# Optimization experiments

Hardware: AMD Instinct MI355X
Metric: run time of the kernel (lower is better)

## Reference

```python
import jax, jax.numpy as jnp
import numpy as np
from jax import lax

BITS = 8  # w_p = a_p = 8 (HAWQ int8)

def _round_ste(x):
    # straight-through round (quant-aware training semantics)
    return x + lax.stop_gradient(jnp.round(x) - x)

def _quant_act(x):
    # QuantAct: symmetric per-tensor activation fake-quant; returns (quantized x, scale)
    n = 2.0 ** (BITS - 1) - 1.0
    sf = jnp.maximum(jnp.max(jnp.abs(x)) / n, 1e-8)
    q = jnp.clip(_round_ste(x / sf), -n, n)
    return q * sf, sf

def _quant_conv(x, w, b, pre_sf, stride, pad):
    # QuantConv2d: per-output-channel symmetric weight quant, integer conv on
    # x/pre_sf with rounded weights, rescale by pre_sf * w_sf. Bias quantized at
    # combined scale. Returns (float output, w_sf) for scale propagation.
    n = 2.0 ** (BITS - 1) - 1.0
    w_sf = jnp.maximum(jnp.max(jnp.abs(w), axis=(1, 2, 3)) / n, 1e-8)
    w_int = _round_ste(w / w_sf[:, None, None, None])
    b_sf = w_sf * pre_sf
    b_int = _round_ste(b / b_sf)
    y = lax.conv_general_dilated(x / pre_sf, w_int, (stride, stride),
                                 [(pad, pad), (pad, pad)],
                                 dimension_numbers=('NCHW', 'OIHW', 'NCHW'))
    return (y + b_int[None, :, None, None]) * b_sf[None, :, None, None], w_sf

def _bn(x, g, b, m, v, eps=1e-5):
    # BatchNorm2d in eval mode (running stats), folded into scale/shift
    inv = g / jnp.sqrt(v + eps)
    return x * inv[None, :, None, None] + (b - m * inv)[None, :, None, None]

def _quant_linear(x, w, b, pre_sf):
    # QuantLinear: per-output-row symmetric weight quant
    n = 2.0 ** (BITS - 1) - 1.0
    w_sf = jnp.maximum(jnp.max(jnp.abs(w), axis=1) / n, 1e-8)
    w_int = _round_ste(w / w_sf[:, None])
    b_sf = w_sf * pre_sf
    b_int = _round_ste(b / b_sf)
    return ((x / pre_sf) @ w_int.T + b_int[None, :]) * b_sf[None, :]

def _forward(x, w0, b0, g0, bb0, m0, v0, w1, b1, g1, bb1, m1, v1,
             w2, b2, g2, bb2, m2, v2, w3, b3, g3, bb3, m3, v3,
             w4, b4, g4, bb4, m4, v4, wd, bd):
    x, psf = _quant_act(x)
    x, _ = _quant_conv(x, w0, b0, psf, 1, 1)   # [B,32,32,32]
    x = _bn(x, g0, bb0, m0, v0)
    x, psf = _quant_act(x)
    x, _ = _quant_conv(x, w1, b1, psf, 1, 0)   # 1x1 -> [B,4,32,32]
    x = _bn(x, g1, bb1, m1, v1)
    x, psf = _quant_act(x)
    x, _ = _quant_conv(x, w2, b2, psf, 2, 1)   # [B,32,16,16]
    x = _bn(x, g2, bb2, m2, v2)
    x, psf = _quant_act(x)
    x, _ = _quant_conv(x, w3, b3, psf, 2, 1)   # [B,32,8,8]
    x = _bn(x, g3, bb3, m3, v3)
    x, psf = _quant_act(x)
    x, _ = _quant_conv(x, w4, b4, psf, 1, 1)   # [B,32,8,8]
    x = _bn(x, g4, bb4, m4, v4)
    x, psf = _quant_act(x)
    x = x.reshape(-1, 2048)                    # 32*8*8 = 2048
    x = _quant_linear(x, wd, bd, psf)          # [B,10]
    return jax.nn.softmax(x, axis=0)           # dim=0 as in original module

def setup_inputs() -> dict:
    key = jax.random.key(0)
    ks = jax.random.split(key, 40)
    B = 1024
    inp = {"x": jax.random.normal(ks[0], (B, 3, 32, 32), jnp.float32)}
    conv_shapes = [(32, 3, 3, 3), (4, 32, 1, 1), (32, 4, 3, 3), (32, 32, 3, 3), (32, 32, 3, 3)]
    for i, s in enumerate(conv_shapes):
        c = s[0]
        inp[f"w{i}"] = jax.random.normal(ks[1 + i], s, jnp.float32) * 0.1
        inp[f"b{i}"] = jax.random.normal(ks[6 + i], (c,), jnp.float32) * 0.01
        inp[f"g{i}"] = 1.0 + 0.1 * jax.random.normal(ks[11 + i], (c,), jnp.float32)
        inp[f"bb{i}"] = 0.1 * jax.random.normal(ks[16 + i], (c,), jnp.float32)
        inp[f"m{i}"] = 0.1 * jax.random.normal(ks[21 + i], (c,), jnp.float32)
        inp[f"v{i}"] = 0.5 + jax.random.uniform(ks[26 + i], (c,), jnp.float32)
    inp["wd"] = jax.random.normal(ks[31], (10, 2048), jnp.float32) * 0.05
    inp["bd"] = jnp.zeros((10,), jnp.float32)
    return inp

def reference(x, w0, b0, g0, bb0, m0, v0, w1, b1, g1, bb1, m1, v1,
              w2, b2, g2, bb2, m2, v2, w3, b3, g3, bb3, m3, v3,
              w4, b4, g4, bb4, m4, v4, wd, bd):
    return _forward(x, w0, b0, g0, bb0, m0, v0, w1, b1, g1, bb1, m1, v1,
                    w2, b2, g2, bb2, m2, v2, w3, b3, g3, bb3, m3, v3,
                    w4, b4, g4, bb4, m4, v4, wd, bd)
```

## Files before the change

kernel.cpp:

```cpp
#include <hip/hip_runtime.h>

#define DI __device__ __forceinline__

constexpr int OFF_W0KT = 384;
constexpr int OFF_W0P  = 1248;
constexpr int OFF_W1I  = 2144;
constexpr int OFF_W2KT = 2272;
constexpr int OFF_W3T  = 3424;
constexpr int OFF_W4T  = 13792;
constexpr int OFF_WDI  = 24160;
constexpr int OFF_WSF0 = 44640;
constexpr int OFF_BNS0 = 44672;
constexpr int OFF_BNB0 = 44704;
constexpr int OFF_WSF1 = 44736;
constexpr int OFF_BNS1 = 44740;
constexpr int OFF_BNB1 = 44744;
constexpr int OFF_WSF2 = 44748;
constexpr int OFF_BNS2 = 44780;
constexpr int OFF_BNB2 = 44812;
constexpr int OFF_WSF3 = 44844;
constexpr int OFF_BNS3 = 44876;
constexpr int OFF_BNB3 = 44908;
constexpr int OFF_WSF4 = 44940;
constexpr int OFF_BNS4 = 44972;
constexpr int OFF_BNB4 = 45004;
constexpr int OFF_WSFD = 45036;
constexpr int OFF_LOG  = 45056;
constexpr int OFF_ACT  = 55296;
constexpr long ACT_A_OFF = OFF_ACT;
constexpr long ACT_B_OFF = OFF_ACT + 8388608L;

DI float quantm(float x, float rsf) {
    float q = rintf(x * rsf);
    return fminf(fmaxf(q, -127.0f), 127.0f);
}
DI float get_sf(const unsigned* umax, int slot) {
    const unsigned* p = umax + slot * 64;
    unsigned m = 0u;
    #pragma unroll
    for (int i = 0; i < 64; ++i) m = m > p[i] ? m : p[i];
    return fmaxf(__uint_as_float(m) / 127.0f, 1e-8f);
}
DI void block_max_atomic(float v, unsigned* dst) {
    __shared__ float redm_[4];
    #pragma unroll
    for (int o = 32; o; o >>= 1) v = fmaxf(v, __shfl_down(v, o, 64));
    int wid = threadIdx.x >> 6;
    if ((threadIdx.x & 63) == 0) redm_[wid] = v;
    __syncthreads();
    if (threadIdx.x == 0) {
        int nw = blockDim.x >> 6;
        float m = redm_[0];
        for (int i = 1; i < nw; ++i) m = fmaxf(m, redm_[i]);
        atomicMax(dst + (blockIdx.x & 63), __float_as_uint(m));
    }
}

struct PrepEntry {
    const float *w, *g, *bb, *m, *v;
    float *wsf, *dst, *dst2, *bns, *bnb;
    int K; int has_bn; int mode;
};
struct PrepAll { PrepEntry e[6]; unsigned* umax; };

__global__ __launch_bounds__(256) void k_prep_all(PrepAll pa) {
    int blk = blockIdx.x;
    if (blk == 142) {
        for (int i = threadIdx.x; i < 384; i += 256) pa.umax[i] = 0u;
        return;
    }
    int layer, oc;
    if      (blk < 32)  { layer = 0; oc = blk; }
    else if (blk < 36)  { layer = 1; oc = blk - 32; }
    else if (blk < 68)  { layer = 2; oc = blk - 36; }
    else if (blk < 100) { layer = 3; oc = blk - 68; }
    else if (blk < 132) { layer = 4; oc = blk - 100; }
    else                { layer = 5; oc = blk - 132; }
    PrepEntry a = pa.e[layer];
    const float* wr = a.w + (long)oc * a.K;
    float mx = 0.f;
    for (int i = threadIdx.x; i < a.K; i += 256) mx = fmaxf(mx, fabsf(wr[i]));
    __shared__ float red[4];
    __shared__ float s_sf;
    #pragma unroll
    for (int o = 32; o; o >>= 1) mx = fmaxf(mx, __shfl_down(mx, o, 64));
    if ((threadIdx.x & 63) == 0) red[threadIdx.x >> 6] = mx;
    __syncthreads();
    if (threadIdx.x == 0) {
        float t = fmaxf(fmaxf(red[0], red[1]), fmaxf(red[2], red[3]));
        t = fmaxf(t / 127.0f, 1e-8f);
        a.wsf[oc] = t; s_sf = t;
        if (a.has_bn) {
            float inv = a.g[oc] / sqrtf(a.v[oc] + 1e-5f);
            a.bns[oc] = inv;
            a.bnb[oc] = a.bb[oc] - a.m[oc] * inv;
        }
    }
    __syncthreads();
    float sf = s_sf;
    for (int i = threadIdx.x; i < a.K; i += 256) {
        float q = rintf(wr[i] / sf);
        if (a.mode == 0) {
            a.dst[(long)oc * a.K + i] = q;
        } else if (a.mode == 1) {
            a.dst[i * 32 + oc] = q;
        } else if (a.mode == 2) {
            a.dst[i * 32 + oc] = q;
            a.dst2[oc * 28 + i] = q;
        } else {
            int ph = i / 72, kk = i - ph * 72;
            a.dst[ph * 2592 + kk * 36 + oc] = q;
        }
    }
    if (a.mode == 2 && threadIdx.x == 0) a.dst2[oc * 28 + 27] = 0.f;
}

__global__ __launch_bounds__(256) void k_absmax(const float4* __restrict__ x, int n4, unsigned* dst) {
    float m = 0.f;
    for (int i = blockIdx.x * blockDim.x + threadIdx.x; i < n4; i += gridDim.x * blockDim.x) {
        float4 t = x[i];
        m = fmaxf(m, fmaxf(fmaxf(fabsf(t.x), fabsf(t.y)), fmaxf(fabsf(t.z), fabsf(t.w))));
    }
    block_max_atomic(m, dst);
}

__global__ __launch_bounds__(256) void k_conv0maxN(
    const float* __restrict__ x, const float* __restrict__ w0kt,
    const float* __restrict__ wsf0, const float* __restrict__ bias0,
    const float* __restrict__ bns0, const float* __restrict__ bnb0,
    const unsigned* __restrict__ umax, unsigned* __restrict__ mout) {
    __shared__ float tile[3 * 18 * 36];
    __shared__ float wlds[27 * 32];
    __shared__ float As[32], Cs[32];
    const int b  = blockIdx.x >> 1;
    const int r0 = (blockIdx.x & 1) * 16;
    const int tid = threadIdx.x;
    const float sfx = get_sf(umax, 0);
    const float rsfx = 1.0f / sfx;
    if (tid < 32) {
        int oc = tid;
        float bsf = wsf0[oc] * sfx;
        float bint = rintf(bias0[oc] / bsf);
        float a = bsf * bns0[oc];
        As[oc] = a;
        Cs[oc] = fmaf(bint, a, bnb0[oc]);
    }
    for (int i = tid; i < 1944; i += 256) tile[i] = 0.f;
    if (tid < 216) ((float4*)wlds)[tid] = ((const float4*)w0kt)[tid];
    __syncthreads();
    const float* xb = x + (long)b * 3072;
    for (int i = tid; i < 1728; i += 256) {
        int ci = i / 576, rem = i - ci * 576;
        int rr = rem >> 5, cc = rem & 31;
        int gr = r0 - 1 + rr;
        if ((unsigned)gr < 32u)
            tile[ci * 648 + rr * 36 + cc + 1] = quantm(xb[ci * 1024 + gr * 32 + cc], rsfx);
    }
    __syncthreads();
    const int oc0  = (tid >> 5) * 4;
    const int pxg  = tid & 31;
    const int row  = pxg >> 1;
    const int wcol = (pxg & 1) * 16;
    float acc[4][16];
    #pragma unroll
    for (int o = 0; o < 4; ++o)
        #pragma unroll
        for (int p = 0; p < 16; ++p) acc[o][p] = 0.f;
    #pragma unroll
    for (int kk = 0; kk < 9; ++kk) {
        int ci = kk / 3, ky = kk - ci * 3;
        const float* rp = tile + ci * 648 + (row + ky) * 36 + wcol;
        float wn[20];
        #pragma unroll
        for (int d = 0; d < 5; ++d) *(float4*)&wn[4 * d] = *(const float4*)&rp[4 * d];
        #pragma unroll
        for (int kx = 0; kx < 3; ++kx) {
            float4 wv = *(const float4*)&wlds[(kk * 3 + kx) * 32 + oc0];
            const float* wf = &wv.x;
            #pragma unroll
            for (int o = 0; o < 4; ++o)
                #pragma unroll
                for (int p = 0; p < 16; ++p)
                    acc[o][p] = fmaf(wn[p + kx], wf[o], acc[o][p]);
        }
    }
    float lmax = 0.f;
    #pragma unroll
    for (int o = 0; o < 4; ++o) {
        float A = As[oc0 + o], C = Cs[oc0 + o];
        #pragma unroll
        for (int p = 0; p < 16; ++p)
            lmax = fmaxf(lmax, fabsf(fmaf(acc[o][p], A, C)));
    }
    block_max_atomic(lmax, mout);
}

__global__ __launch_bounds__(256) void k_conv01n(
    const float* __restrict__ x, const float* __restrict__ w0p,
    const float* __restrict__ wsf0, const float* __restrict__ bias0,
    const float* __restrict__ bns0, const float* __restrict__ bnb0,
    const float* __restrict__ w1i,
    const float* __restrict__ wsf1, const float* __restrict__ bias1,
    const float* __restrict__ bns1, const float* __restrict__ bnb1,
    const unsigned* __restrict__ umax, unsigned* __restrict__ mout,
    float* __restrict__ out) {
    __shared__ float tile[3672];
    __shared__ float wls0[896];
    __shared__ float wls1[128];
    __shared__ float Aq[32], Cq[32];
    __shared__ float A1s[4], C1s[4];
    const int b   = blockIdx.x;
    const int tid = threadIdx.x;
    const float sfx = get_sf(umax, 0);
    const float rsfx = 1.0f / sfx;
    const float sf1 = get_sf(umax, 1);
    const float rsf1 = 1.0f / sf1;
    if (tid < 32) {
        int oc = tid;
        float bsf = wsf0[oc] * sfx;
        float bint = rintf(bias0[oc] / bsf);
        float a = bsf * bns0[oc];
        float c = fmaf(bint, a, bnb0[oc]);
        Aq[oc] = a * rsf1;
        Cq[oc] = c * rsf1;
    }
    if (tid >= 64 && tid < 68) {
        int oc = tid - 64;
        float bsf = wsf1[oc] * sf1;
        float bint = rintf(bias1[oc] / bsf);
        float a = bsf * bns1[oc];
        A1s[oc] = a;
        C1s[oc] = fmaf(bint, a, bnb1[oc]);
    }
    for (int i = tid; i < 3672; i += 256) tile[i] = 0.f;
    if (tid < 224) ((float4*)wls0)[tid] = ((const float4*)w0p)[tid];
    if (tid >= 128 && tid < 256) {
        int j = tid - 128;
        wls1[(j & 31) * 4 + (j >> 5)] = w1i[j];
    }
    __syncthreads();
    const float* xb = x + (long)b * 3072;
    for (int i = tid; i < 3072; i += 256) {
        int ci = i >> 10, px = i & 1023;
        int iy = px >> 5, ix = px & 31;
        tile[ci * 1224 + (iy + 1) * 36 + (ix + 1)] = quantm(xb[i], rsfx);
    }
    __syncthreads();
    const int h   = tid >> 3;
    const int w0c = (tid & 7) * 4;
    float win[3][3][6];
    #pragma unroll
    for (int ci = 0; ci < 3; ++ci)
        #pragma unroll
        for (int ky = 0; ky < 3; ++ky) {
            const int base = ci * 1224 + (h + ky) * 36 + w0c;
            *(float4*)&win[ci][ky][0] = *(const float4*)&tile[base];
            *(float2*)&win[ci][ky][4] = *(const float2*)&tile[base + 4];
        }
    float acc1[4][4];
    #pragma unroll
    for (int o = 0; o < 4; ++o)
        #pragma unroll
        for (int p = 0; p < 4; ++p) acc1[o][p] = 0.f;
    #pragma unroll 2
    for (int oc = 0; oc < 32; ++oc) {
        float wreg[28];
        const float4* wp4 = (const float4*)&wls0[oc * 28];
        #pragma unroll
        for (int d = 0; d < 7; ++d) *(float4*)&wreg[4 * d] = wp4[d];
        float a0 = 0.f, a1 = 0.f, a2 = 0.f, a3 = 0.f;
        #pragma unroll
        for (int ci = 0; ci < 3; ++ci)
            #pragma unroll
            for (int ky = 0; ky < 3; ++ky)
                #pragma unroll
                for (int kx = 0; kx < 3; ++kx) {
                    float wv = wreg[ci * 9 + ky * 3 + kx];
                    a0 = fmaf(win[ci][ky][kx + 0], wv, a0);
                    a1 = fmaf(win[ci][ky][kx + 1], wv, a1);
                    a2 = fmaf(win[ci][ky][kx + 2], wv, a2);
                    a3 = fmaf(win[ci][ky][kx + 3], wv, a3);
                }
        float A = Aq[oc], C = Cq[oc];
        float q0 = fminf(fmaxf(rintf(fmaf(a0, A, C)), -127.0f), 127.0f);
        float q1 = fminf(fmaxf(rintf(fmaf(a1, A, C)), -127.0f), 127.0f);
        float q2 = fminf(fmaxf(rintf(fmaf(a2, A, C)), -127.0f), 127.0f);
        float q3 = fminf(fmaxf(rintf(fmaf(a3, A, C)), -127.0f), 127.0f);
        const float4 w1v = *(const float4*)&wls1[oc * 4];
        acc1[0][0] = fmaf(q0, w1v.x, acc1[0][0]); acc1[0][1] = fmaf(q1, w1v.x, acc1[0][1]);
        acc1[0][2] = fmaf(q2, w1v.x, acc1[0][2]); acc1[0][3] = fmaf(q3, w1v.x, acc1[0][3]);
        acc1[1][0] = fmaf(q0, w1v.y, acc1[1][0]); acc1[1][1] = fmaf(q1, w1v.y, acc1[1][1]);
        acc1[1][2] = fmaf(q2, w1v.y, acc1[1][2]); acc1[1][3] = fmaf(q3, w1v.y, acc1[1][3]);
        acc1[2][0] = fmaf(q0, w1v.z, acc1[2][0]); acc1[2][1] = fmaf(q1, w1v.z, acc1[2][1]);
        acc1[2][2] = fmaf(q2, w1v.z, acc1[2][2]); acc1[2][3] = fmaf(q3, w1v.z, acc1[2][3]);
        acc1[3][0] = fmaf(q0, w1v.w, acc1[3][0]); acc1[3][1] = fmaf(q1, w1v.w, acc1[3][1]);
        acc1[3][2] = fmaf(q2, w1v.w, acc1[3][2]); acc1[3][3] = fmaf(q3, w1v.w, acc1[3][3]);
    }
    float lmax = 0.f;
    float* ob = out + (long)b * 4096 + h * 32 + w0c;
    #pragma unroll
    for (int o = 0; o < 4; ++o) {
        float y0 = fmaf(acc1[o][0], A1s[o], C1s[o]);
        float y1 = fmaf(acc1[o][1], A1s[o], C1s[o]);
        float y2 = fmaf(acc1[o][2], A1s[o], C1s[o]);
        float y3 = fmaf(acc1[o][3], A1s[o], C1s[o]);
        lmax = fmaxf(lmax, fmaxf(fmaxf(fabsf(y0), fabsf(y1)), fmaxf(fabsf(y2), fabsf(y3))));
        float4 r4; r4.x = y0; r4.y = y1; r4.z = y2; r4.w = y3;
        *(float4*)&ob[o * 1024] = r4;
    }
    block_max_atomic(lmax, mout);
}

__global__ __launch_bounds__(256) void k_conv2c(
    const float* __restrict__ inp, const float* __restrict__ w2kt,
    const float* __restrict__ wsf, const float* __restrict__ bias,
    const float* __restrict__ bns, const float* __restrict__ bnb,
    const unsigned* __restrict__ umax, unsigned* __restrict__ mout,
    float* __restrict__ out) {
    __shared__ float tile[4 * 34 * 36];
    __shared__ float wlds[36 * 32];
    __shared__ float As[32], Cs[32];
    const int tid = threadIdx.x;
    const float sf = get_sf(umax, 2);
    const float rsf = 1.0f / sf;
    if (tid < 32) {
        int oc = tid;
        float bsf = wsf[oc] * sf;
        float bint = rintf(bias[oc] / bsf);
        float a = bsf * bns[oc];
        As[oc] = a;
        Cs[oc] = fmaf(bint, a, bnb[oc]);
    }
    for (int i = tid; i < 4896; i += 256) tile[i] = 0.f;
    for (int i = tid; i < 288; i += 256) ((float4*)wlds)[i] = ((const float4*)w2kt)[i];
    __syncthreads();
    const float* ib = inp + (long)blockIdx.x * 4096;
    for (int i = tid; i < 4096; i += 256) {
        int ci = i >> 10, px = i & 1023;
        int iy = px >> 5, ix = px & 31;
        tile[ci * 1224 + (iy + 1) * 36 + (ix + 1)] = quantm(ib[i], rsf);
    }
    __syncthreads();
    const int oc0 = (tid >> 6) * 8;
    const int pxq = tid & 63;
    const int h = pxq >> 2, c = pxq & 3;
    float acc[8][4];
    #pragma unroll
    for (int k = 0; k < 8; ++k)
        #pragma unroll
        for (int p = 0; p < 4; ++p) acc[k][p] = 0.f;
    #pragma unroll
    for (int ci = 0; ci < 4; ++ci) {
        #pragma unroll
        for (int ky = 0; ky < 3; ++ky) {
            const float* rp = tile + ci * 1224 + (2 * h + ky) * 36 + 8 * c;
            float wn[12];
            #pragma unroll
            for (int d = 0; d < 3; ++d) *(float4*)&wn[4 * d] = *(const float4*)&rp[4 * d];
            #pragma unroll
            for (int kx = 0; kx < 3; ++kx) {
                const float* wp = &wlds[(ci * 9 + ky * 3 + kx) * 32 + oc0];
                float4 wa = *(const float4*)&wp[0];
                float4 wb = *(const float4*)&wp[4];
                float wf[8] = {wa.x, wa.y, wa.z, wa.w, wb.x, wb.y, wb.z, wb.w};
                #pragma unroll
                for (int k = 0; k < 8; ++k)
                    #pragma unroll
                    for (int p = 0; p < 4; ++p)
                        acc[k][p] = fmaf(wn[2 * p + kx], wf[k], acc[k][p]);
            }
        }
    }
    float lmax = 0.f;
    float* ob = out + (long)blockIdx.x * 8192;
    #pragma unroll
    for (int k = 0; k < 8; ++k) {
        int oc = oc0 + k;
        float A = As[oc], C = Cs[oc];
        float4 r;
        float* rp = &r.x;
        #pragma unroll
        for (int p = 0; p < 4; ++p) {
            float y = fmaf(acc[k][p], A, C);
            rp[p] = y;
            lmax = fmaxf(lmax, fabsf(y));
        }
        *(float4*)&ob[oc * 256 + h * 16 + c * 4] = r;
    }
    block_max_atomic(lmax, mout);
}

template<int HIN, int S>
__global__ __launch_bounds__(256) void k_conv34d(
    const float* __restrict__ inp, const float* __restrict__ wt,
    const float* __restrict__ wsf, const float* __restrict__ bias,
    const float* __restrict__ bns, const float* __restrict__ bnb,
    const unsigned* __restrict__ umax, int slot, unsigned* __restrict__ mout,
    float* __restrict__ out) {
    constexpr int ROWS = HIN + 2;
    constexpr int RS   = (S == 2) ? 20 : 12;
    constexpr int TI   = 8 * ROWS * RS;
    constexpr int PIX  = HIN * HIN;
    constexpr int PSH  = (HIN == 16) ? 8 : 6;
    constexpr int HSH  = (HIN == 16) ? 4 : 3;
    constexpr int NELT = 2 * 8 * PIX;
    constexpr int WINW = (S == 2) ? 12 : 8;
    constexpr int ND   = (S == 2) ? 3 : 2;
    __shared__ float tile[2 * TI];
    __shared__ float wlds[2592];
    __shared__ float As[32], Cs[32];
    const int tid  = threadIdx.x;
    const int imgl = tid >> 7;
    const int ocg  = (tid >> 4) & 7;
    const int pxq  = tid & 15;
    const int h = pxq >> 1, c = pxq & 1;
    const float sf = get_sf(umax, slot);
    const float rsf = 1.0f / sf;
    if (tid < 32) {
        int oc = tid;
        float bsf = wsf[oc] * sf;
        float bint = rintf(bias[oc] / bsf);
        float a = bsf * bns[oc];
        As[oc] = a;
        Cs[oc] = fmaf(bint, a, bnb[oc]);
    }
    for (int i = tid; i < 2 * TI; i += 256) tile[i] = 0.f;
    float acc[4][4];
    #pragma unroll
    for (int k = 0; k < 4; ++k)
        #pragma unroll
        for (int p = 0; p < 4; ++p) acc[k][p] = 0.f;
    const float* ib = inp + (long)blockIdx.x * 2 * 32 * PIX;
    const float4* wt4 = (const float4*)wt;
    for (int ph = 0; ph < 4; ++ph) {
        __syncthreads();
        for (int i = tid; i < NELT; i += 256) {
            int im = i >> (PSH + 3);
            int ci = (i >> PSH) & 7;
            int px = i & (PIX - 1);
            int iy = px >> HSH, ix = px & (HIN - 1);
            tile[im * TI + ci * (ROWS * RS) + (iy + 1) * RS + (ix + 1)] =
                quantm(ib[(long)((im * 32 + ph * 8 + ci) << PSH) + px], rsf);
        }
        for (int i = tid; i < 648; i += 256) ((float4*)wlds)[i] = wt4[ph * 648 + i];
        __syncthreads();
        const int tbo = imgl * TI;
        #pragma unroll
        for (int ci = 0; ci < 8; ++ci) {
            float win[3][WINW];
            #pragma unroll
            for (int ky = 0; ky < 3; ++ky) {
                const int base = tbo + ci * (ROWS * RS) + (S * h + ky) * RS + S * 4 * c;
                #pragma unroll
                for (int d = 0; d < ND; ++d)
                    *(float4*)&win[ky][4 * d] = *(const float4*)&tile[base + 4 * d];
            }
            #pragma unroll
            for (int ky = 0; ky < 3; ++ky)
                #pragma unroll
                for (int kx = 0; kx < 3; ++kx) {
                    int j = ky * 3 + kx;
                    float4 wv = *(const float4*)&wlds[(ci * 9 + j) * 36 + ocg * 4];
                    float x0 = win[ky][S * 0 + kx];
                    float x1 = win[ky][S * 1 + kx];
                    float x2 = win[ky][S * 2 + kx];
                    float x3 = win[ky][S * 3 + kx];
                    acc[0][0] = fmaf(x0, wv.x, acc[0][0]); acc[0][1] = fmaf(x1, wv.x, acc[0][1]);
                    acc[0][2] = fmaf(x2, wv.x, acc[0][2]); acc[0][3] = fmaf(x3, wv.x, acc[0][3]);
                    acc[1][0] = fmaf(x0, wv.y, acc[1][0]); acc[1][1] = fmaf(x1, wv.y, acc[1][1]);
                    acc[1][2] = fmaf(x2, wv.y, acc[1][2]); acc[1][3] = fmaf(x3, wv.y, acc[1][3]);
                    acc[2][0] = fmaf(x0, wv.z, acc[2][0]); acc[2][1] = fmaf(x1, wv.z, acc[2][1]);
                    acc[2][2] = fmaf(x2, wv.z, acc[2][2]); acc[2][3] = fmaf(x3, wv.z, acc[2][3]);
                    acc[3][0] = fmaf(x0, wv.w, acc[3][0]); acc[3][1] = fmaf(x1, wv.w, acc[3][1]);
                    acc[3][2] = fmaf(x2, wv.w, acc[3][2]); acc[3][3] = fmaf(x3, wv.w, acc[3][3]);
                }
        }
    }
    float lmax = 0.f;
    long imgg = (long)blockIdx.x * 2 + imgl;
    #pragma unroll
    for (int k = 0; k < 4; ++k) {
        int oc = ocg * 4 + k;
        float A = As[oc], C = Cs[oc];
        float y0 = fmaf(acc[k][0], A, C);
        float y1 = fmaf(acc[k][1], A, C);
        float y2 = fmaf(acc[k][2], A, C);
        float y3 = fmaf(acc[k][3], A, C);
        lmax = fmaxf(lmax, fmaxf(fmaxf(fabsf(y0), fabsf(y1)), fmaxf(fabsf(y2), fabsf(y3))));
        float4 r4; r4.x = y0; r4.y = y1; r4.z = y2; r4.w = y3;
        *(float4*)&out[(imgg * 32 + oc) * 64 + h * 8 + c * 4] = r4;
    }
    block_max_atomic(lmax, mout);
}

__global__ __launch_bounds__(256) void k_fc(
    const float* __restrict__ act, const float* __restrict__ wdi,
    const float* __restrict__ wsfd, const float* __restrict__ bd,
    const unsigned* __restrict__ umax, float* __restrict__ logits) {
    int b = blockIdx.x;
    float sf = get_sf(umax, 5);
    float rsf = 1.0f / sf;
    const float* ab = act + (long)b * 2048;
    float acc[10];
    #pragma unroll
    for (int c = 0; c < 10; ++c) acc[c] = 0.f;
    #pragma unroll
    for (int k = 0; k < 8; ++k) {
        int j = threadIdx.x + 256 * k;
        float q = quantm(ab[j], rsf);
        #pragma unroll
        for (int c = 0; c < 10; ++c) acc[c] = fmaf(q, wdi[c * 2048 + j], acc[c]);
    }
    #pragma unroll
    for (int c = 0; c < 10; ++c)
        #pragma unroll
        for (int o = 32; o; o >>= 1) acc[c] += __shfl_down(acc[c], o, 64);
    __shared__ float red[4][10];
    int wid = threadIdx.x >> 6;
    if ((threadIdx.x & 63) == 0)
        #pragma unroll
        for (int c = 0; c < 10; ++c) red[wid][c] = acc[c];
    __syncthreads();
    if (threadIdx.x < 10) {
        int c = threadIdx.x;
        float s = red[0][c] + red[1][c] + red[2][c] + red[3][c];
        float bsf = wsfd[c] * sf;
        float bint = rintf(bd[c] / bsf);
        logits[b * 10 + c] = (s + bint) * bsf;
    }
}

__global__ __launch_bounds__(256) void k_softmax(const float* __restrict__ logits, float* __restrict__ out) {
    int c = blockIdx.x;
    float v0 = logits[(threadIdx.x +   0) * 10 + c];
    float v1 = logits[(threadIdx.x + 256) * 10 + c];
    float v2 = logits[(threadIdx.x + 512) * 10 + c];
    float v3 = logits[(threadIdx.x + 768) * 10 + c];
    float mx = fmaxf(fmaxf(v0, v1), fmaxf(v2, v3));
    __shared__ float redm[4];
    __shared__ float reds[4];
    #pragma unroll
    for (int o = 32; o; o >>= 1) mx = fmaxf(mx, __shfl_down(mx, o, 64));
    if ((threadIdx.x & 63) == 0) redm[threadIdx.x >> 6] = mx;
    __syncthreads();
    mx = fmaxf(fmaxf(redm[0], redm[1]), fmaxf(redm[2], redm[3]));
    float e0 = expf(v0 - mx), e1 = expf(v1 - mx), e2 = expf(v2 - mx), e3 = expf(v3 - mx);
    float s = (e0 + e1) + (e2 + e3);
    #pragma unroll
    for (int o = 32; o; o >>= 1) s += __shfl_down(s, o, 64);
    if ((threadIdx.x & 63) == 0) reds[threadIdx.x >> 6] = s;
    __syncthreads();
    s = reds[0] + reds[1] + reds[2] + reds[3];
    out[(threadIdx.x +   0) * 10 + c] = e0 / s;
    out[(threadIdx.x + 256) * 10 + c] = e1 / s;
    out[(threadIdx.x + 512) * 10 + c] = e2 / s;
    out[(threadIdx.x + 768) * 10 + c] = e3 / s;
}

extern "C" void kernel_launch(void* const* d_in, const int* in_sizes, int n_in,
                              void* d_out, int out_size, void* d_ws, size_t ws_size,
                              hipStream_t stream) {
    (void)in_sizes; (void)n_in; (void)out_size; (void)ws_size;
    const float* x = (const float*)d_in[0];
    const float *w[5], *bia[5], *g[5], *bb[5], *m[5], *v[5];
    for (int i = 0; i < 5; ++i) {
        w[i]   = (const float*)d_in[1 + 6 * i + 0];
        bia[i] = (const float*)d_in[1 + 6 * i + 1];
        g[i]   = (const float*)d_in[1 + 6 * i + 2];
        bb[i]  = (const float*)d_in[1 + 6 * i + 3];
        m[i]   = (const float*)d_in[1 + 6 * i + 4];
        v[i]   = (const float*)d_in[1 + 6 * i + 5];
    }
    const float* wd = (const float*)d_in[31];
    const float* bd = (const float*)d_in[32];
    float* ws = (float*)d_ws;
    unsigned* umax = (unsigned*)ws;
    float* out = (float*)d_out;

    float* w0kt = ws + OFF_W0KT;
    float* w0p  = ws + OFF_W0P;
    float* w1i  = ws + OFF_W1I;
    float* w2kt = ws + OFF_W2KT;
    float* w3t  = ws + OFF_W3T;
    float* w4t  = ws + OFF_W4T;
    float* wdi  = ws + OFF_WDI;
    float* wsf0 = ws + OFF_WSF0; float* bns0 = ws + OFF_BNS0; float* bnb0 = ws + OFF_BNB0;
    float* wsf1 = ws + OFF_WSF1; float* bns1 = ws + OFF_BNS1; float* bnb1 = ws + OFF_BNB1;
    float* wsf2 = ws + OFF_WSF2; float* bns2 = ws + OFF_BNS2; float* bnb2 = ws + OFF_BNB2;
    float* wsf3 = ws + OFF_WSF3; float* bns3 = ws + OFF_BNS3; float* bnb3 = ws + OFF_BNB3;
    float* wsf4 = ws + OFF_WSF4; float* bns4 = ws + OFF_BNS4; float* bnb4 = ws + OFF_BNB4;
    float* wsfd = ws + OFF_WSFD;
    float* logits = ws + OFF_LOG;
    float* actA = ws + ACT_A_OFF;
    float* actB = ws + ACT_B_OFF;

    PrepAll pa;
    pa.umax = umax;
    const float* ww[6] = {w[0], w[1], w[2], w[3], w[4], wd};
    float* wsfp[6] = {wsf0, wsf1, wsf2, wsf3, wsf4, wsfd};
    float* dstp[6] = {w0kt, w1i, w2kt, w3t, w4t, wdi};
    float* dst2p[6] = {w0p, nullptr, nullptr, nullptr, nullptr, nullptr};
    float* bnsp[6] = {bns0, bns1, bns2, bns3, bns4, nullptr};
    float* bnbp[6] = {bnb0, bnb1, bnb2, bnb3, bnb4, nullptr};
    int Ks[6]   = {27, 32, 36, 288, 288, 2048};
    int modes[6] = {2, 0, 1, 3, 3, 0};
    for (int i = 0; i < 6; ++i) {
        pa.e[i].w = ww[i];
        pa.e[i].g = (i < 5) ? g[i] : nullptr;
        pa.e[i].bb = (i < 5) ? bb[i] : nullptr;
        pa.e[i].m = (i < 5) ? m[i] : nullptr;
        pa.e[i].v = (i < 5) ? v[i] : nullptr;
        pa.e[i].wsf = wsfp[i];
        pa.e[i].dst = dstp[i];
        pa.e[i].dst2 = dst2p[i];
        pa.e[i].bns = bnsp[i];
        pa.e[i].bnb = bnbp[i];
        pa.e[i].K = Ks[i];
        pa.e[i].has_bn = (i < 5) ? 1 : 0;
        pa.e[i].mode = modes[i];
    }

    hipLaunchKernelGGL(k_prep_all, dim3(143), dim3(256), 0, stream, pa);
    hipLaunchKernelGGL(k_absmax, dim3(1024), dim3(256), 0, stream,
                       (const float4*)x, 1024 * 3 * 32 * 32 / 4, umax + 0 * 64);
    hipLaunchKernelGGL(k_conv0maxN, dim3(2048), dim3(256), 0, stream,
                       x, w0kt, wsf0, bia[0], bns0, bnb0, umax, umax + 1 * 64);
    hipLaunchKernelGGL(k_conv01n, dim3(1024), dim3(256), 0, stream,
                       x, w0p, wsf0, bia[0], bns0, bnb0,
                       w1i, wsf1, bia[1], bns1, bnb1, umax, umax + 2 * 64, actB);
    hipLaunchKernelGGL(k_conv2c, dim3(1024), dim3(256), 0, stream,
                       actB, w2kt, wsf2, bia[2], bns2, bnb2, umax, umax + 3 * 64, actA);
    hipLaunchKernelGGL((k_conv34d<16, 2>), dim3(512), dim3(256), 0, stream,
                       actA, w3t, wsf3, bia[3], bns3, bnb3, umax, 3, umax + 4 * 64, actB);
    hipLaunchKernelGGL((k_conv34d<8, 1>),  dim3(512), dim3(256), 0, stream,
                       actB, w4t, wsf4, bia[4], bns4, bnb4, umax, 4, umax + 5 * 64, actA);
    hipLaunchKernelGGL(k_fc, dim3(1024), dim3(256), 0, stream, actA, wdi, wsfd, bd, umax, logits);
    hipLaunchKernelGGL(k_softmax, dim3(10), dim3(256), 0, stream, logits, out);
}
```

Before: 162.4 us.

## Fuse input absmax into prep kernel and give conv3/4 threads two output rows

The input abs-max reduction moves into the prep kernel as 256 extra blocks. Each block writes its partial max to its own slot instead of using atomics, and the conv kernels that read it reduce over all 256 slots. This removes one kernel launch. Separately, the conv3/conv4 kernels now run with 128 threads per block, and each thread computes two output rows, so loaded input windows are reused across rows. The cost is more registers per thread and fewer threads per block.

```diff
diff --git a/kernel.cpp b/kernel.cpp
--- a/kernel.cpp
+++ b/kernel.cpp
@@ -2,31 +2,31 @@
 
 #define DI __device__ __forceinline__
 
-constexpr int OFF_W0KT = 384;
-constexpr int OFF_W0P  = 1248;
-constexpr int OFF_W1I  = 2144;
-constexpr int OFF_W2KT = 2272;
-constexpr int OFF_W3T  = 3424;
-constexpr int OFF_W4T  = 13792;
-constexpr int OFF_WDI  = 24160;
-constexpr int OFF_WSF0 = 44640;
-constexpr int OFF_BNS0 = 44672;
-constexpr int OFF_BNB0 = 44704;
-constexpr int OFF_WSF1 = 44736;
-constexpr int OFF_BNS1 = 44740;
-constexpr int OFF_BNB1 = 44744;
-constexpr int OFF_WSF2 = 44748;
-constexpr int OFF_BNS2 = 44780;
-constexpr int OFF_BNB2 = 44812;
-constexpr int OFF_WSF3 = 44844;
-constexpr int OFF_BNS3 = 44876;
-constexpr int OFF_BNB3 = 44908;
-constexpr int OFF_WSF4 = 44940;
-constexpr int OFF_BNS4 = 44972;
-constexpr int OFF_BNB4 = 45004;
-constexpr int OFF_WSFD = 45036;
-constexpr int OFF_LOG  = 45056;
-constexpr int OFF_ACT  = 55296;
+constexpr int OFF_W0KT = 576;
+constexpr int OFF_W0P  = 1440;
+constexpr int OFF_W1I  = 2336;
+constexpr int OFF_W2KT = 2464;
+constexpr int OFF_W3T  = 3616;
+constexpr int OFF_W4T  = 13984;
+constexpr int OFF_WDI  = 24352;
+constexpr int OFF_WSF0 = 44832;
+constexpr int OFF_BNS0 = 44864;
+constexpr int OFF_BNB0 = 44896;
+constexpr int OFF_WSF1 = 44928;
+constexpr int OFF_BNS1 = 44932;
+constexpr int OFF_BNB1 = 44936;
+constexpr int OFF_WSF2 = 44940;
+constexpr int OFF_BNS2 = 44972;
+constexpr int OFF_BNB2 = 45004;
+constexpr int OFF_WSF3 = 45036;
+constexpr int OFF_BNS3 = 45068;
+constexpr int OFF_BNB3 = 45100;
+constexpr int OFF_WSF4 = 45132;
+constexpr int OFF_BNS4 = 45164;
+constexpr int OFF_BNB4 = 45196;
+constexpr int OFF_WSFD = 45228;
+constexpr int OFF_LOG  = 45248;
+constexpr int OFF_ACT  = 55488;
 constexpr long ACT_A_OFF = OFF_ACT;
 constexpr long ACT_B_OFF = OFF_ACT + 8388608L;
 
@@ -34,8 +34,14 @@
     float q = rintf(x * rsf);
     return fminf(fmaxf(q, -127.0f), 127.0f);
 }
+DI float get_sf0(const unsigned* umax) {
+    unsigned m = 0u;
+    #pragma unroll
+    for (int i = 0; i < 256; ++i) m = m > umax[i] ? m : umax[i];
+    return fmaxf(__uint_as_float(m) / 127.0f, 1e-8f);
+}
 DI float get_sf(const unsigned* umax, int slot) {
-    const unsigned* p = umax + slot * 64;
+    const unsigned* p = umax + 192 + slot * 64;
     unsigned m = 0u;
     #pragma unroll
     for (int i = 0; i < 64; ++i) m = m > p[i] ? m : p[i];
@@ -61,12 +67,30 @@
     float *wsf, *dst, *dst2, *bns, *bnb;
     int K; int has_bn; int mode;
 };
-struct PrepAll { PrepEntry e[6]; unsigned* umax; };
+struct PrepAll { PrepEntry e[6]; unsigned* umax; const float4* x; };
 
 __global__ __launch_bounds__(256) void k_prep_all(PrepAll pa) {
     int blk = blockIdx.x;
+    __shared__ float red[4];
+    __shared__ float s_sf;
+    if (blk >= 143) {
+        int j = blk - 143;
+        float m = 0.f;
+        for (int i = j * 256 + threadIdx.x; i < 786432; i += 65536) {
+            float4 t = pa.x[i];
+            m = fmaxf(m, fmaxf(fmaxf(fabsf(t.x), fabsf(t.y)), fmaxf(fabsf(t.z), fabsf(t.w))));
+        }
+        #pragma unroll
+        for (int o = 32; o; o >>= 1) m = fmaxf(m, __shfl_down(m, o, 64));
+        int wid = threadIdx.x >> 6;
+        if ((threadIdx.x & 63) == 0) red[wid] = m;
+        __syncthreads();
+        if (threadIdx.x == 0)
+            pa.umax[j] = __float_as_uint(fmaxf(fmaxf(red[0], red[1]), fmaxf(red[2], red[3])));
+        return;
+    }
     if (blk == 142) {
-        for (int i = threadIdx.x; i < 384; i += 256) pa.umax[i] = 0u;
+        for (int i = threadIdx.x; i < 320; i += 256) pa.umax[256 + i] = 0u;
         return;
     }
     int layer, oc;
@@ -80,8 +104,6 @@
     const float* wr = a.w + (long)oc * a.K;
     float mx = 0.f;
     for (int i = threadIdx.x; i < a.K; i += 256) mx = fmaxf(mx, fabsf(wr[i]));
-    __shared__ float red[4];
-    __shared__ float s_sf;
     #pragma unroll
     for (int o = 32; o; o >>= 1) mx = fmaxf(mx, __shfl_down(mx, o, 64));
     if ((threadIdx.x & 63) == 0) red[threadIdx.x >> 6] = mx;
@@ -115,15 +137,6 @@
     if (a.mode == 2 && threadIdx.x == 0) a.dst2[oc * 28 + 27] = 0.f;
 }
 
-__global__ __launch_bounds__(256) void k_absmax(const float4* __restrict__ x, int n4, unsigned* dst) {
-    float m = 0.f;
-    for (int i = blockIdx.x * blockDim.x + threadIdx.x; i < n4; i += gridDim.x * blockDim.x) {
-        float4 t = x[i];
-        m = fmaxf(m, fmaxf(fmaxf(fabsf(t.x), fabsf(t.y)), fmaxf(fabsf(t.z), fabsf(t.w))));
-    }
-    block_max_atomic(m, dst);
-}
-
 __global__ __launch_bounds__(256) void k_conv0maxN(
     const float* __restrict__ x, const float* __restrict__ w0kt,
     const float* __restrict__ wsf0, const float* __restrict__ bias0,
@@ -135,7 +148,7 @@
     const int b  = blockIdx.x >> 1;
     const int r0 = (blockIdx.x & 1) * 16;
     const int tid = threadIdx.x;
-    const float sfx = get_sf(umax, 0);
+    const float sfx = get_sf0(umax);
     const float rsfx = 1.0f / sfx;
     if (tid < 32) {
         int oc = tid;
@@ -211,7 +224,7 @@
     __shared__ float A1s[4], C1s[4];
     const int b   = blockIdx.x;
     const int tid = threadIdx.x;
-    const float sfx = get_sf(umax, 0);
+    const float sfx = get_sf0(umax);
     const float rsfx = 1.0f / sfx;
     const float sf1 = get_sf(umax, 1);
     const float rsf1 = 1.0f / sf1;
@@ -391,7 +404,7 @@
 }
 
 template<int HIN, int S>
-__global__ __launch_bounds__(256) void k_conv34d(
+__global__ __launch_bounds__(128) void k_conv34e(
     const float* __restrict__ inp, const float* __restrict__ wt,
     const float* __restrict__ wsf, const float* __restrict__ bias,
     const float* __restrict__ bns, const float* __restrict__ bnb,
@@ -404,16 +417,16 @@
     constexpr int PSH  = (HIN == 16) ? 8 : 6;
     constexpr int HSH  = (HIN == 16) ? 4 : 3;
     constexpr int NELT = 2 * 8 * PIX;
-    constexpr int WINW = (S == 2) ? 12 : 8;
-    constexpr int ND   = (S == 2) ? 3 : 2;
+    constexpr int NR   = S + 3;
+    constexpr int NCF  = (S == 2) ? 3 : 2;
     __shared__ float tile[2 * TI];
     __shared__ float wlds[2592];
     __shared__ float As[32], Cs[32];
     const int tid  = threadIdx.x;
-    const int imgl = tid >> 7;
-    const int ocg  = (tid >> 4) & 7;
-    const int pxq  = tid & 15;
-    const int h = pxq >> 1, c = pxq & 1;
+    const int imgl = tid >> 6;
+    const int ocg  = (tid >> 3) & 7;
+    const int pxq  = tid & 7;
+    const int h2 = pxq >> 1, c = pxq & 1;
     const float sf = get_sf(umax, slot);
     const float rsf = 1.0f / sf;
     if (tid < 32) {
@@ -424,17 +437,19 @@
         As[oc] = a;
         Cs[oc] = fmaf(bint, a, bnb[oc]);
     }
-    for (int i = tid; i < 2 * TI; i += 256) tile[i] = 0.f;
-    float acc[4][4];
+    for (int i = tid; i < 2 * TI; i += 128) tile[i] = 0.f;
+    float acc[4][2][4];
     #pragma unroll
     for (int k = 0; k < 4; ++k)
         #pragma unroll
-        for (int p = 0; p < 4; ++p) acc[k][p] = 0.f;
+        for (int r = 0; r < 2; ++r)
+            #pragma unroll
+            for (int p = 0; p < 4; ++p) acc[k][r][p] = 0.f;
     const float* ib = inp + (long)blockIdx.x * 2 * 32 * PIX;
     const float4* wt4 = (const float4*)wt;
     for (int ph = 0; ph < 4; ++ph) {
         __syncthreads();
-        for (int i = tid; i < NELT; i += 256) {
+        for (int i = tid; i < NELT; i += 128) {
             int im = i >> (PSH + 3);
             int ci = (i >> PSH) & 7;
             int px = i & (PIX - 1);
@@ -442,37 +457,48 @@
             tile[im * TI + ci * (ROWS * RS) + (iy + 1) * RS + (ix + 1)] =
                 quantm(ib[(long)((im * 32 + ph * 8 + ci) << PSH) + px], rsf);
         }
-        for (int i = tid; i < 648; i += 256) ((float4*)wlds)[i] = wt4[ph * 648 + i];
+        for (int i = tid; i < 648; i += 128) ((float4*)wlds)[i] = wt4[ph * 648 + i];
         __syncthreads();
         const int tbo = imgl * TI;
         #pragma unroll
         for (int ci = 0; ci < 8; ++ci) {
-            float win[3][WINW];
+            float win[NR][NCF * 4];
             #pragma unroll
-            for (int ky = 0; ky < 3; ++ky) {
-                const int base = tbo + ci * (ROWS * RS) + (S * h + ky) * RS + S * 4 * c;
+            for (int rr = 0; rr < NR; ++rr) {
+                const int base = tbo + ci * (ROWS * RS) + (2 * S * h2 + rr) * RS + S * 4 * c;
                 #pragma unroll
-                for (int d = 0; d < ND; ++d)
-                    *(float4*)&win[ky][4 * d] = *(const float4*)&tile[base + 4 * d];
+                for (int d = 0; d < NCF; ++d)
+                    *(float4*)&win[rr][4 * d] = *(const float4*)&tile[base + 4 * d];
             }
             #pragma unroll
             for (int ky = 0; ky < 3; ++ky)
                 #pragma unroll
                 for (int kx = 0; kx < 3; ++kx) {
-                    int j = ky * 3 + kx;
-                    float4 wv = *(const float4*)&wlds[(ci * 9 + j) * 36 + ocg * 4];
-                    float x0 = win[ky][S * 0 + kx];
-                    float x1 = win[ky][S * 1 + kx];
-                    float x2 = win[ky][S * 2 + kx];
-                    float x3 = win[ky][S * 3 + kx];
-                    acc[0][0] = fmaf(x0, wv.x, acc[0][0]); acc[0][1] = fmaf(x1, wv.x, acc[0][1]);
-                    acc[0][2] = fmaf(x2, wv.x, acc[0][2]); acc[0][3] = fmaf(x3, wv.x, acc[0][3]);
-                    acc[1][0] = fmaf(x0, wv.y, acc[1][0]); acc[1][1] = fmaf(x1, wv.y, acc[1][1]);
-                    acc[1][2] = fmaf(x2, wv.y, acc[1][2]); acc[1][3] = fmaf(x3, wv.y, acc[1][3]);
-                    acc[2][0] = fmaf(x0, wv.z, acc[2][0]); acc[2][1] = fmaf(x1, wv.z, acc[2][1]);
-                    acc[2][2] = fmaf(x2, wv.z, acc[2][2]); acc[2][3] = fmaf(x3, wv.z, acc[2][3]);
-                    acc[3][0] = fmaf(x0, wv.w, acc[3][0]); acc[3][1] = fmaf(x1, wv.w, acc[3][1]);
-                    acc[3][2] = fmaf(x2, wv.w, acc[3][2]); acc[3][3] = fmaf(x3, wv.w, acc[3][3]);
+                    float4 wv = *(const float4*)&wlds[(ci * 9 + ky * 3 + kx) * 36 + ocg * 4];
+                    float x00 = win[ky][S * 0 + kx];
+                    float x01 = win[ky][S * 1 + kx];
+                    float x02 = win[ky][S * 2 + kx];
+                    float x03 = win[ky][S * 3 + kx];
+                    float x10 = win[S + ky][S * 0 + kx];
+                    float x11 = win[S + ky][S * 1 + kx];
+                    float x12 = win[S + ky][S * 2 + kx];
+                    float x13 = win[S + ky][S * 3 + kx];
+                    acc[0][0][0] = fmaf(x00, wv.x, acc[0][0][0]); acc[0][0][1] = fmaf(x01, wv.x, acc[0][0][1]);
+                    acc[0][0][2] = fmaf(x02, wv.x, acc[0][0][2]); acc[0][0][3] = fmaf(x03, wv.x, acc[0][0][3]);
+                    acc[0][1][0] = fmaf(x10, wv.x, acc[0][1][0]); acc[0][1][1] = fmaf(x11, wv.x, acc[0][1][1]);
+                    acc[0][1][2] = fmaf(x12, wv.x, acc[0][1][2]); acc[0][1][3] = fmaf(x13, wv.x, acc[0][1][3]);
+                    acc[1][0][0] = fmaf(x00, wv.y, acc[1][0][0]); acc[1][0][1] = fmaf(x01, wv.y, acc[1][0][1]);
+                    acc[1][0][2] = fmaf(x02, wv.y, acc[1][0][2]); acc[1][0][3] = fmaf(x03, wv.y, acc[1][0][3]);
+                    acc[1][1][0] = fmaf(x10, wv.y, acc[1][1][0]); acc[1][1][1] = fmaf(x11, wv.y, acc[1][1][1]);
+                    acc[1][1][2] = fmaf(x12, wv.y, acc[1][1][2]); acc[1][1][3] = fmaf(x13, wv.y, acc[1][1][3]);
+                    acc[2][0][0] = fmaf(x00, wv.z, acc[2][0][0]); acc[2][0][1] = fmaf(x01, wv.z, acc[2][0][1]);
+                    acc[2][0][2] = fmaf(x02, wv.z, acc[2][0][2]); acc[2][0][3] = fmaf(x03, wv.z, acc[2][0][3]);
+                    acc[2][1][0] = fmaf(x10, wv.z, acc[2][1][0]); acc[2][1][1] = fmaf(x11, wv.z, acc[2][1][1]);
+                    acc[2][1][2] = fmaf(x12, wv.z, acc[2][1][2]); acc[2][1][3] = fmaf(x13, wv.z, acc[2][1][3]);
+                    acc[3][0][0] = fmaf(x00, wv.w, acc[3][0][0]); acc[3][0][1] = fmaf(x01, wv.w, acc[3][0][1]);
+                    acc[3][0][2] = fmaf(x02, wv.w, acc[3][0][2]); acc[3][0][3] = fmaf(x03, wv.w, acc[3][0][3]);
+                    acc[3][1][0] = fmaf(x10, wv.w, acc[3][1][0]); acc[3][1][1] = fmaf(x11, wv.w, acc[3][1][1]);
+                    acc[3][1][2] = fmaf(x12, wv.w, acc[3][1][2]); acc[3][1][3] = fmaf(x13, wv.w, acc[3][1][3]);
                 }
         }
     }
@@ -482,13 +508,16 @@
     for (int k = 0; k < 4; ++k) {
         int oc = ocg * 4 + k;
         float A = As[oc], C = Cs[oc];
-        float y0 = fmaf(acc[k][0], A, C);
-        float y1 = fmaf(acc[k][1], A, C);
-        float y2 = fmaf(acc[k][2], A, C);
-        float y3 = fmaf(acc[k][3], A, C);
-        lmax = fmaxf(lmax, fmaxf(fmaxf(fabsf(y0), fabsf(y1)), fmaxf(fabsf(y2), fabsf(y3))));
-        float4 r4; r4.x = y0; r4.y = y1; r4.z = y2; r4.w = y3;
-        *(float4*)&out[(imgg * 32 + oc) * 64 + h * 8 + c * 4] = r4;
+        #pragma unroll
+        for (int r = 0; r < 2; ++r) {
+            float y0 = fmaf(acc[k][r][0], A, C);
+            float y1 = fmaf(acc[k][r][1], A, C);
+            float y2 = fmaf(acc[k][r][2], A, C);
+            float y3 = fmaf(acc[k][r][3], A, C);
+            lmax = fmaxf(lmax, fmaxf(fmaxf(fabsf(y0), fabsf(y1)), fmaxf(fabsf(y2), fabsf(y3))));
+            float4 r4; r4.x = y0; r4.y = y1; r4.z = y2; r4.w = y3;
+            *(float4*)&out[(imgg * 32 + oc) * 64 + (2 * h2 + r) * 8 + c * 4] = r4;
+        }
     }
     block_max_atomic(lmax, mout);
 }
@@ -596,6 +625,7 @@
 
     PrepAll pa;
     pa.umax = umax;
+    pa.x = (const float4*)x;
     const float* ww[6] = {w[0], w[1], w[2], w[3], w[4], wd};
     float* wsfp[6] = {wsf0, wsf1, wsf2, wsf3, wsf4, wsfd};
     float* dstp[6] = {w0kt, w1i, w2kt, w3t, w4t, wdi};
@@ -620,20 +650,18 @@
         pa.e[i].mode = modes[i];
     }
 
-    hipLaunchKernelGGL(k_prep_all, dim3(143), dim3(256), 0, stream, pa);
-    hipLaunchKernelGGL(k_absmax, dim3(1024), dim3(256), 0, stream,
-                       (const float4*)x, 1024 * 3 * 32 * 32 / 4, umax + 0 * 64);
+    hipLaunchKernelGGL(k_prep_all, dim3(399), dim3(256), 0, stream, pa);
     hipLaunchKernelGGL(k_conv0maxN, dim3(2048), dim3(256), 0, stream,
-                       x, w0kt, wsf0, bia[0], bns0, bnb0, umax, umax + 1 * 64);
+                       x, w0kt, wsf0, bia[0], bns0, bnb0, umax, umax + 256);
     hipLaunchKernelGGL(k_conv01n, dim3(1024), dim3(256), 0, stream,
                        x, w0p, wsf0, bia[0], bns0, bnb0,
-                       w1i, wsf1, bia[1], bns1, bnb1, umax, umax + 2 * 64, actB);
+                       w1i, wsf1, bia[1], bns1, bnb1, umax, umax + 320, actB);
     hipLaunchKernelGGL(k_conv2c, dim3(1024), dim3(256), 0, stream,
-                       actB, w2kt, wsf2, bia[2], bns2, bnb2, umax, umax + 3 * 64, actA);
-    hipLaunchKernelGGL((k_conv34d<16, 2>), dim3(512), dim3(256), 0, stream,
-                       actA, w3t, wsf3, bia[3], bns3, bnb3, umax, 3, umax + 4 * 64, actB);
-    hipLaunchKernelGGL((k_conv34d<8, 1>),  dim3(512), dim3(256), 0, stream,
-                       actB, w4t, wsf4, bia[4], bns4, bnb4, umax, 4, umax + 5 * 64, actA);
+                       actB, w2kt, wsf2, bia[2], bns2, bnb2, umax, umax + 384, actA);
+    hipLaunchKernelGGL((k_conv34e<16, 2>), dim3(512), dim3(128), 0, stream,
+                       actA, w3t, wsf3, bia[3], bns3, bnb3, umax, 3, umax + 448, actB);
+    hipLaunchKernelGGL((k_conv34e<8, 1>),  dim3(512), dim3(128), 0, stream,
+                       actB, w4t, wsf4, bia[4], bns4, bnb4, umax, 4, umax + 512, actA);
     hipLaunchKernelGGL(k_fc, dim3(1024), dim3(256), 0, stream, actA, wdi, wsfd, bd, umax, logits);
     hipLaunchKernelGGL(k_softmax, dim3(10), dim3(256), 0, stream, logits, out);
 }
```

Measured after the change: 178.7 us. +10.0%, slower.
